# Optimization experiments

Hardware: AMD Instinct MI355X
Metric: run time of the kernel (lower is better)

## Reference

```python
import jax, jax.numpy as jnp
import numpy as np

B, H, LQ, LK, DK = 4, 8, 256, 256, 64

def setup_inputs() -> dict:
    key = jax.random.key(0)
    ks = jax.random.split(key, 9)
    s = 1.0 / np.sqrt(DK)
    return {
        "q": jax.random.normal(ks[0], (B, H, LQ, DK), jnp.float32),
        "k": jax.random.normal(ks[1], (B, H, LK, DK), jnp.float32),
        "v": jax.random.normal(ks[2], (B, H, LK, DK), jnp.float32),
        "Wq_w": jax.random.uniform(ks[3], (DK, DK), jnp.float32, -s, s),
        "Wq_b": jax.random.uniform(ks[4], (DK,), jnp.float32, -s, s),
        "Wk_w": jax.random.uniform(ks[5], (DK, DK), jnp.float32, -s, s),
        "Wk_b": jax.random.uniform(ks[6], (DK,), jnp.float32, -s, s),
        "vs_w": jax.random.uniform(ks[7], (1, DK), jnp.float32, -s, s),
        "vs_b": jax.random.uniform(ks[8], (1,), jnp.float32, -s, s),
    }

def reference(q, k, v, Wq_w, Wq_b, Wk_w, Wk_b, vs_w, vs_b):
    # Additive (Bahdanau) attention; dropout is identity at eval time.
    qp = jnp.einsum('bhqd,ed->bhqe', q, Wq_w) + Wq_b          # [B,H,Lq,d_k]
    kp = jnp.einsum('bhkd,ed->bhke', k, Wk_w) + Wk_b          # [B,H,Lk,d_k]
    # Broadcast add -> tanh -> linear projection to scalar score
    feat = jnp.tanh(qp[:, :, :, None, :] + kp[:, :, None, :, :])  # [B,H,Lq,Lk,d_k]
    scores = jnp.einsum('bhqkd,d->bhqk', feat, vs_w[0]) + vs_b[0]  # [B,H,Lq,Lk]
    attn = jax.nn.softmax(scores, axis=-1)
    output = jnp.einsum('bhqk,bhkd->bhqd', attn, v)
    return output, attn
```

## Files before the change

### kernel.cpp

```cpp
#include <hip/hip_runtime.h>

#define B_ 4
#define H_ 8
#define LQ_ 256
#define LK_ 256
#define DK_ 64
#define BH_ (B_*H_)
#define NROWS (BH_*LQ_)
#define QT 8

__global__ __launch_bounds__(256) void proj_kernel(
    const float* __restrict__ qin, const float* __restrict__ kin,
    const float* __restrict__ Wq, const float* __restrict__ bq,
    const float* __restrict__ Wk, const float* __restrict__ bk,
    float* __restrict__ eq, float* __restrict__ ekt)
{
    const int which = blockIdx.x >> 8;
    const int rb    = (blockIdx.x & 255) * 32;
    const float* in   = which ? kin : qin;
    const float* W    = which ? Wk  : Wq;
    const float* bias = which ? bk  : bq;

    __shared__ float in_s[32*68];
    __shared__ float w_s[64*68];
    const int tid = threadIdx.x;

    {
        const float4* g = (const float4*)(in + rb*64);
        #pragma unroll
        for (int p = 0; p < 2; ++p) {
            int f = tid + p*256;
            float4 x = g[f];
            *(float4*)&in_s[(f>>4)*68 + (f&15)*4] = x;
        }
    }
    {
        const float4* g = (const float4*)W;
        #pragma unroll
        for (int p = 0; p < 4; ++p) {
            int f = tid + p*256;
            float4 x = g[f];
            *(float4*)&w_s[(f>>4)*68 + (f&15)*4] = x;
        }
    }
    __syncthreads();

    const int r  = tid >> 3;
    const int gg = tid & 7;
    float acc[8];
    #pragma unroll
    for (int i = 0; i < 8; ++i) acc[i] = 0.f;

    #pragma unroll
    for (int j = 0; j < 16; ++j) {
        float4 x = *(const float4*)&in_s[r*68 + j*4];
        #pragma unroll
        for (int i = 0; i < 8; ++i) {
            float4 w = *(const float4*)&w_s[(gg + i*8)*68 + j*4];
            acc[i] = fmaf(w.x, x.x, acc[i]);
            acc[i] = fmaf(w.y, x.y, acc[i]);
            acc[i] = fmaf(w.z, x.z, acc[i]);
            acc[i] = fmaf(w.w, x.w, acc[i]);
        }
    }
    const float C2 = 2.8853900817779268f;
    if (which == 0) {
        float* orow = eq + (rb + r)*64;
        #pragma unroll
        for (int i = 0; i < 8; ++i) {
            const int e = gg + i*8;
            orow[e] = __builtin_amdgcn_exp2f((acc[i] + bias[e]) * C2);
        }
    } else {
        const int bh = rb >> 8;
        const int kk = (rb & 255) + r;
        float* ob = ekt + bh*64*256 + kk;
        #pragma unroll
        for (int i = 0; i < 8; ++i) {
            const int e = gg + i*8;
            ob[e*256] = __builtin_amdgcn_exp2f((acc[i] + bias[e]) * C2);
        }
    }
}

__global__ __launch_bounds__(256) void score_softmax_pv_kernel(
    const float* __restrict__ eq, const float* __restrict__ ekt,
    const float* __restrict__ vs_w, const float* __restrict__ vs_b,
    const float* __restrict__ v,
    float* __restrict__ attn, float* __restrict__ out)
{
    const int bh = blockIdx.x >> 5;
    const int qt = blockIdx.x & 31;
    const int t  = threadIdx.x;
    const int lane = t & 63, wid = t >> 6;

    const float L2E = 1.4426950408889634f;

    __shared__ float reds[QT][4];
    __shared__ float a_s[QT*256];
    __shared__ float p_s[4*QT*64];

    const float* ekb = ekt + bh*64*256 + t;
    float e0 = ekb[0], e1 = ekb[256], e2 = ekb[512], e3 = ekb[768];

    const float* qrow = eq + (bh*LQ_ + qt*QT)*64;

    float S = vs_b[0];
    #pragma unroll
    for (int j = 0; j < 16; ++j) {
        float4 w = *(const float4*)&vs_w[j*4];
        S += (w.x + w.y) + (w.z + w.w);
    }

    float sc[QT] = {0.f,0.f,0.f,0.f,0.f,0.f,0.f,0.f};
    #pragma unroll 1
    for (int c = 0; c < 16; ++c) {
        const int nc = ((c+1) & 15) * 4;
        float n0 = ekb[(nc+0)*256], n1 = ekb[(nc+1)*256];
        float n2 = ekb[(nc+2)*256], n3 = ekb[(nc+3)*256];
        float4 wv = *(const float4*)&vs_w[c*4];
        #pragma unroll
        for (int q = 0; q < QT; ++q) {
            float4 qv = *(const float4*)&qrow[q*64 + c*4];
            float x0 = fmaf(qv.x, e0, 1.f);
            float x1 = fmaf(qv.y, e1, 1.f);
            float x2 = fmaf(qv.z, e2, 1.f);
            float x3 = fmaf(qv.w, e3, 1.f);
            float d01 = x0*x1, d23 = x2*x3;
            float n01 = fmaf(wv.x, x1, wv.y*x0);
            float n23 = fmaf(wv.z, x3, wv.w*x2);
            float N   = fmaf(n01, d23, n23*d01);
            sc[q] = fmaf(N, __builtin_amdgcn_rcpf(d01*d23), sc[q]);
        }
        e0 = n0; e1 = n1; e2 = n2; e3 = n3;
    }

    float p[QT];
    #pragma unroll
    for (int q = 0; q < QT; ++q) {
        p[q] = __builtin_amdgcn_exp2f((S - 2.f*sc[q]) * L2E);
        float s = p[q];
        #pragma unroll
        for (int off = 32; off; off >>= 1) s += __shfl_xor(s, off, 64);
        if (lane == 0) reds[q][wid] = s;
    }
    __syncthreads();
    #pragma unroll
    for (int q = 0; q < QT; ++q) {
        float s = (reds[q][0] + reds[q][1]) + (reds[q][2] + reds[q][3]);
        float a = p[q] * __builtin_amdgcn_rcpf(s);
        attn[(bh*LQ_ + qt*QT + q)*LK_ + t] = a;
        a_s[q*256 + t] = a;
    }
    __syncthreads();

    {
        float acc[QT] = {0.f,0.f,0.f,0.f,0.f,0.f,0.f,0.f};
        const float* vb = v + (bh*LK_ + wid*64)*DK_ + lane;
        #pragma unroll 2
        for (int k4 = 0; k4 < 16; ++k4) {
            float v0 = vb[(k4*4+0)*64];
            float v1 = vb[(k4*4+1)*64];
            float v2 = vb[(k4*4+2)*64];
            float v3 = vb[(k4*4+3)*64];
            #pragma unroll
            for (int q = 0; q < QT; ++q) {
                float4 a4 = *(const float4*)&a_s[q*256 + wid*64 + k4*4];
                acc[q] = fmaf(a4.x, v0, acc[q]);
                acc[q] = fmaf(a4.y, v1, acc[q]);
                acc[q] = fmaf(a4.z, v2, acc[q]);
                acc[q] = fmaf(a4.w, v3, acc[q]);
            }
        }
        #pragma unroll
        for (int q = 0; q < QT; ++q) p_s[wid*512 + q*64 + lane] = acc[q];
    }
    __syncthreads();
    {
        float* ob = out + (bh*LQ_ + qt*QT)*DK_;
        #pragma unroll
        for (int h = 0; h < 2; ++h) {
            int idx = t + h*256;
            float s = (p_s[idx] + p_s[512 + idx]) + (p_s[1024 + idx] + p_s[1536 + idx]);
            ob[idx] = s;
        }
    }
}

extern "C" void kernel_launch(void* const* d_in, const int* in_sizes, int n_in,
                              void* d_out, int out_size, void* d_ws, size_t ws_size,
                              hipStream_t stream) {
    const float* q    = (const float*)d_in[0];
    const float* k    = (const float*)d_in[1];
    const float* v    = (const float*)d_in[2];
    const float* Wq_w = (const float*)d_in[3];
    const float* Wq_b = (const float*)d_in[4];
    const float* Wk_w = (const float*)d_in[5];
    const float* Wk_b = (const float*)d_in[6];
    const float* vs_w = (const float*)d_in[7];
    const float* vs_b = (const float*)d_in[8];

    float* out  = (float*)d_out;
    float* attn = out + B_*H_*LQ_*DK_;
    float* eq   = (float*)d_ws;
    float* ekt  = eq + NROWS*64;

    proj_kernel<<<512, 256, 0, stream>>>(q, k, Wq_w, Wq_b, Wk_w, Wk_b, eq, ekt);
    score_softmax_pv_kernel<<<BH_*(LQ_/QT), 256, 0, stream>>>(
        eq, ekt, vs_w, vs_b, v, attn, out);
}
```

Baseline: 101.8 us.

## Use packed FP32 FMA/MUL instructions in score and PV loops with permuted layouts

Rewrites the score inner loop and the attention-times-V accumulation to use v_pk_fma_f32 and v_pk_mul_f32 through inline asm, so each instruction handles two fp32 lanes. To make the pairs line up, the projection kernel writes eq with a permuted feature order and emits a permuted copy of vs_w into the workspace. The aim is to roughly halve VALU instruction count in the compute-bound score loop. Risks include forcing q and w operands into SGPR constraints (qv comes from global loads, which may need readfirstlane or fail to be uniform), a slight change in accumulation order, and the inline asm blocking compiler scheduling.

Result: no change. 102.7 us (+0.8%).

```diff
diff --git a/kernel.cpp b/kernel.cpp
--- a/kernel.cpp
+++ b/kernel.cpp
@@ -9,11 +9,41 @@
 #define NROWS (BH_*LQ_)
 #define QT 8
 
+
+typedef float f32x2 __attribute__((ext_vector_type(2)));
+typedef float f32x4 __attribute__((ext_vector_type(4)));
+
+__device__ __forceinline__ f32x2 pk_fma_vsv(f32x2 a, f32x2 b_sgpr, f32x2 c) {
+    f32x2 d;
+    asm("v_pk_fma_f32 %0, %1, %2, %3" : "=v"(d) : "v"(a), "s"(b_sgpr), "v"(c));
+    return d;
+}
+__device__ __forceinline__ f32x2 pk_mul_vs(f32x2 a, f32x2 b_sgpr) {
+    f32x2 d;
+    asm("v_pk_mul_f32 %0, %1, %2" : "=v"(d) : "v"(a), "s"(b_sgpr));
+    return d;
+}
+__device__ __forceinline__ f32x2 pk_mul_vv(f32x2 a, f32x2 b) {
+    f32x2 d;
+    asm("v_pk_mul_f32 %0, %1, %2" : "=v"(d) : "v"(a), "v"(b));
+    return d;
+}
+__device__ __forceinline__ f32x2 pk_fma_vvv(f32x2 a, f32x2 b, f32x2 c) {
+    f32x2 d;
+    asm("v_pk_fma_f32 %0, %1, %2, %3" : "=v"(d) : "v"(a), "v"(b), "v"(c));
+    return d;
+}
+
+__device__ __forceinline__ int perm4(int e) {
+    return (e & 0x3C) | (((e & 1) << 1) | ((e >> 1) & 1));
+}
+
 __global__ __launch_bounds__(256) void proj_kernel(
     const float* __restrict__ qin, const float* __restrict__ kin,
     const float* __restrict__ Wq, const float* __restrict__ bq,
     const float* __restrict__ Wk, const float* __restrict__ bk,
-    float* __restrict__ eq, float* __restrict__ ekt)
+    const float* __restrict__ vs_w,
+    float* __restrict__ eq, float* __restrict__ ekt, float* __restrict__ wvp)
 {
     const int which = blockIdx.x >> 8;
     const int rb    = (blockIdx.x & 255) * 32;
@@ -21,6 +51,11 @@
     const float* W    = which ? Wk  : Wq;
     const float* bias = which ? bk  : bq;
 
+    if (blockIdx.x == 0 && threadIdx.x < 64) {
+        const int s = threadIdx.x;
+        wvp[s] = vs_w[perm4(s)];
+    }
+
     __shared__ float in_s[32*68];
     __shared__ float w_s[64*68];
     const int tid = threadIdx.x;
@@ -69,7 +104,7 @@
         #pragma unroll
         for (int i = 0; i < 8; ++i) {
             const int e = gg + i*8;
-            orow[e] = __builtin_amdgcn_exp2f((acc[i] + bias[e]) * C2);
+            orow[perm4(e)] = __builtin_amdgcn_exp2f((acc[i] + bias[e]) * C2);
         }
     } else {
         const int bh = rb >> 8;
@@ -85,7 +120,7 @@
 
 __global__ __launch_bounds__(256) void score_softmax_pv_kernel(
     const float* __restrict__ eq, const float* __restrict__ ekt,
-    const float* __restrict__ vs_w, const float* __restrict__ vs_b,
+    const float* __restrict__ wvp, const float* __restrict__ vs_b,
     const float* __restrict__ v,
     float* __restrict__ attn, float* __restrict__ out)
 {
@@ -101,38 +136,41 @@
     __shared__ float p_s[4*QT*64];
 
     const float* ekb = ekt + bh*64*256 + t;
-    float e0 = ekb[0], e1 = ekb[256], e2 = ekb[512], e3 = ekb[768];
+    f32x2 eP, eQ;
+    eP.x = ekb[0];   eQ.x = ekb[256];
+    eP.y = ekb[512]; eQ.y = ekb[768];
 
     const float* qrow = eq + (bh*LQ_ + qt*QT)*64;
 
     float S = vs_b[0];
     #pragma unroll
     for (int j = 0; j < 16; ++j) {
-        float4 w = *(const float4*)&vs_w[j*4];
+        f32x4 w = *(const f32x4*)&wvp[j*4];
         S += (w.x + w.y) + (w.z + w.w);
     }
+
+    const f32x2 one2 = {1.f, 1.f};
 
     float sc[QT] = {0.f,0.f,0.f,0.f,0.f,0.f,0.f,0.f};
     #pragma unroll 1
     for (int c = 0; c < 16; ++c) {
         const int nc = ((c+1) & 15) * 4;
-        float n0 = ekb[(nc+0)*256], n1 = ekb[(nc+1)*256];
-        float n2 = ekb[(nc+2)*256], n3 = ekb[(nc+3)*256];
-        float4 wv = *(const float4*)&vs_w[c*4];
+        f32x2 nP, nQ;
+        nP.x = ekb[(nc+0)*256]; nQ.x = ekb[(nc+1)*256];
+        nP.y = ekb[(nc+2)*256]; nQ.y = ekb[(nc+3)*256];
+        f32x4 wv = *(const f32x4*)&wvp[c*4];
         #pragma unroll
         for (int q = 0; q < QT; ++q) {
-            float4 qv = *(const float4*)&qrow[q*64 + c*4];
-            float x0 = fmaf(qv.x, e0, 1.f);
-            float x1 = fmaf(qv.y, e1, 1.f);
-            float x2 = fmaf(qv.z, e2, 1.f);
-            float x3 = fmaf(qv.w, e3, 1.f);
-            float d01 = x0*x1, d23 = x2*x3;
-            float n01 = fmaf(wv.x, x1, wv.y*x0);
-            float n23 = fmaf(wv.z, x3, wv.w*x2);
-            float N   = fmaf(n01, d23, n23*d01);
-            sc[q] = fmaf(N, __builtin_amdgcn_rcpf(d01*d23), sc[q]);
-        }
-        e0 = n0; e1 = n1; e2 = n2; e3 = n3;
+            f32x4 qv = *(const f32x4*)&qrow[q*64 + c*4];
+            f32x2 P  = pk_fma_vsv(eP, qv.xy, one2);
+            f32x2 Q  = pk_fma_vsv(eQ, qv.zw, one2);
+            f32x2 D  = pk_mul_vv(P, Q);
+            f32x2 T  = pk_mul_vs(P, wv.zw);
+            f32x2 Np = pk_fma_vsv(Q, wv.xy, T);
+            float N  = fmaf(Np.x, D.y, Np.y * D.x);
+            sc[q] = fmaf(N, __builtin_amdgcn_rcpf(D.x * D.y), sc[q]);
+        }
+        eP = nP; eQ = nQ;
     }
 
     float p[QT];
@@ -155,25 +193,27 @@
     __syncthreads();
 
     {
-        float acc[QT] = {0.f,0.f,0.f,0.f,0.f,0.f,0.f,0.f};
+        f32x2 accP[QT];
+        #pragma unroll
+        for (int q = 0; q < QT; ++q) accP[q] = (f32x2){0.f, 0.f};
         const float* vb = v + (bh*LK_ + wid*64)*DK_ + lane;
         #pragma unroll 2
         for (int k4 = 0; k4 < 16; ++k4) {
-            float v0 = vb[(k4*4+0)*64];
-            float v1 = vb[(k4*4+1)*64];
-            float v2 = vb[(k4*4+2)*64];
-            float v3 = vb[(k4*4+3)*64];
+            f32x2 V01, V23;
+            V01.x = vb[(k4*4+0)*64];
+            V01.y = vb[(k4*4+1)*64];
+            V23.x = vb[(k4*4+2)*64];
+            V23.y = vb[(k4*4+3)*64];
             #pragma unroll
             for (int q = 0; q < QT; ++q) {
-                float4 a4 = *(const float4*)&a_s[q*256 + wid*64 + k4*4];
-                acc[q] = fmaf(a4.x, v0, acc[q]);
-                acc[q] = fmaf(a4.y, v1, acc[q]);
-                acc[q] = fmaf(a4.z, v2, acc[q]);
-                acc[q] = fmaf(a4.w, v3, acc[q]);
+                f32x4 a4 = *(const f32x4*)&a_s[q*256 + wid*64 + k4*4];
+                accP[q] = pk_fma_vvv(a4.xy, V01, accP[q]);
+                accP[q] = pk_fma_vvv(a4.zw, V23, accP[q]);
             }
         }
         #pragma unroll
-        for (int q = 0; q < QT; ++q) p_s[wid*512 + q*64 + lane] = acc[q];
+        for (int q = 0; q < QT; ++q)
+            p_s[wid*512 + q*64 + lane] = accP[q].x + accP[q].y;
     }
     __syncthreads();
     {
@@ -204,8 +244,10 @@
     float* attn = out + B_*H_*LQ_*DK_;
     float* eq   = (float*)d_ws;
     float* ekt  = eq + NROWS*64;
-
-    proj_kernel<<<512, 256, 0, stream>>>(q, k, Wq_w, Wq_b, Wk_w, Wk_b, eq, ekt);
+    float* wvp  = ekt + NROWS*64;
+
+    proj_kernel<<<512, 256, 0, stream>>>(q, k, Wq_w, Wq_b, Wk_w, Wk_b, vs_w,
+                                         eq, ekt, wvp);
     score_softmax_pv_kernel<<<BH_*(LQ_/QT), 256, 0, stream>>>(
-        eq, ekt, vs_w, vs_b, v, attn, out);
-}
+        eq, ekt, wvp, vs_b, v, attn, out);
+}
```
